# Optimization experiments

Hardware: AMD Instinct MI355X
Metric: run time of the kernel (lower is better)

Reference implementation:

```python
import jax, jax.numpy as jnp
import numpy as np

B, N, D = 4, 2048, 1024
H, HD = 16, 64          # heads, head dim
ROT = 64                # rotary dims (full head)
SCALE = HD ** -0.5


def _rotate_half(x):
    # interleaved pair rotation: (c r) with r=2 -> (-x2, x1)
    x = x.reshape(x.shape[:-1] + (-1, 2))
    x1, x2 = x[..., 0], x[..., 1]
    return jnp.stack((-x2, x1), axis=-1).reshape(x.shape[:-2] + (-1,))


def _rope(t, pos_enc):
    # t: [b,h,n,c], pos_enc: [1,n,rot] -> broadcast over heads
    pe = pos_enc[:, None, : t.shape[-2], :]          # [1,1,n,rot]
    t_rot, t_pass = t[..., :ROT], t[..., ROT:]
    t_rot = t_rot * jnp.cos(pe) + _rotate_half(t_rot) * jnp.sin(pe)
    return jnp.concatenate((t_rot, t_pass), axis=-1)


def setup_inputs() -> dict:
    key = jax.random.key(0)
    ks = jax.random.split(key, 16)
    s = 0.02
    return {
        "query": jax.random.normal(ks[0], (B, N, D), jnp.float32),
        "key": jax.random.normal(ks[1], (B, N, D), jnp.float32),
        "value": jax.random.normal(ks[2], (B, N, D), jnp.float32),
        "pad_mask": jax.random.randint(ks[3], (B, N), 0, 2) > 0,
        "pos_enc": jax.random.uniform(ks[4], (1, N, ROT), jnp.float32),
        "Wq": jax.random.normal(ks[5], (D, D), jnp.float32) * s,
        "bq": jnp.zeros((D,), jnp.float32),
        "Wk": jax.random.normal(ks[6], (D, D), jnp.float32) * s,
        "bk": jnp.zeros((D,), jnp.float32),
        "Wv": jax.random.normal(ks[7], (D, D), jnp.float32) * s,
        "bv": jnp.zeros((D,), jnp.float32),
        "Wo": jax.random.normal(ks[8], (D, D), jnp.float32) * s,
        "bo": jnp.zeros((D,), jnp.float32),
    }


def reference(query, key, value, pad_mask, pos_enc, Wq, bq, Wk, bk, Wv, bv, Wo, bo):
    def split_heads(x):
        return x.reshape(x.shape[0], x.shape[1], H, HD).transpose(0, 2, 1, 3)  # b h n c

    q = split_heads(query @ Wq + bq) * SCALE
    k = split_heads(key @ Wk + bk)
    v = split_heads(value @ Wv + bv)

    q = _rope(q, pos_enc)
    k = _rope(k, pos_enc)

    attn = jnp.einsum("bhic,bhjc->bhij", q, k)
    neg = -jnp.finfo(attn.dtype).max
    attn = jnp.where(pad_mask[:, None, None, :], neg, attn)
    attn = jax.nn.softmax(attn, axis=-1)

    o = jnp.einsum("bhij,bhjc->bhic", attn, v)
    o = o.transpose(0, 2, 1, 3).reshape(o.shape[0], o.shape[2], H * HD)  # b n (h c)
    return o @ Wo + bo
```

## Files before the change

### kernel.cpp

```cpp
#include <hip/hip_runtime.h>

#define B_ 4
#define N_ 2048
#define D_ 1024
#define H_ 16
#define HD_ 64
#define QSCALE_ 0.18033688011112042f

typedef __bf16 bf16x8 __attribute__((ext_vector_type(8)));
typedef float f32x4 __attribute__((ext_vector_type(4)));

#if __has_builtin(__builtin_amdgcn_exp2f)
#define EXP2(x) __builtin_amdgcn_exp2f(x)
#else
#define EXP2(x) exp2f(x)
#endif

__device__ __forceinline__ f32x4 mfma16(bf16x8 a, bf16x8 b, f32x4 c) {
    return __builtin_amdgcn_mfma_f32_16x16x32_bf16(a, b, c, 0, 0, 0);
}

__device__ __forceinline__ void gload16(const void* g, void* l) {
    __builtin_amdgcn_global_load_lds(
        (const __attribute__((address_space(1))) void*)g,
        (__attribute__((address_space(3))) void*)l, 16, 0, 0);
}

__device__ __forceinline__ unsigned pack2(float x, float y) {
    __bf16 a = (__bf16)x, b = (__bf16)y;
    unsigned ua = __builtin_bit_cast(unsigned short, a);
    unsigned ub = __builtin_bit_cast(unsigned short, b);
    return ua | (ub << 16);
}

__global__ __launch_bounds__(256) void pre_kernel(
    const float* __restrict__ q, const float* __restrict__ k, const float* __restrict__ v,
    __bf16* __restrict__ xb,
    const float* __restrict__ W0, const float* __restrict__ W1,
    const float* __restrict__ W2, const float* __restrict__ W3,
    __bf16* __restrict__ T0, __bf16* __restrict__ T1,
    __bf16* __restrict__ T2, __bf16* __restrict__ T3,
    const float* __restrict__ pe, const int* __restrict__ mask,
    unsigned* __restrict__ cstab, float* __restrict__ maskf)
{
    const int y = blockIdx.y;
    const int x = blockIdx.x;
    const int t = threadIdx.x;

    if (y < 3) {
        const float* src = (y == 0) ? q : (y == 1) ? k : v;
        __bf16* dst = xb + (size_t)y * 8388608;
        size_t i = ((size_t)x * 256 + t) * 8;
        float4 a = *(const float4*)(src + i);
        float4 b = *(const float4*)(src + i + 4);
        bf16x8 o;
        o[0] = (__bf16)a.x; o[1] = (__bf16)a.y; o[2] = (__bf16)a.z; o[3] = (__bf16)a.w;
        o[4] = (__bf16)b.x; o[5] = (__bf16)b.y; o[6] = (__bf16)b.z; o[7] = (__bf16)b.w;
        *(bf16x8*)(dst + i) = o;
        return;
    }
    if (x < 1024) {
        const int which = x >> 8;
        const float* W = (which == 0) ? W0 : (which == 1) ? W1 : (which == 2) ? W2 : W3;
        __bf16* Wt = (which == 0) ? T0 : (which == 1) ? T1 : (which == 2) ? T2 : T3;
        const int k0 = ((x >> 4) & 15) * 64, n0 = (x & 15) * 64;
        __shared__ float T[64][65];
#pragma unroll
        for (int i = 0; i < 4; ++i) {
            int row = i * 16 + (t >> 4);
            int c4 = (t & 15) * 4;
            float4 vv = *(const float4*)(W + (size_t)(k0 + row) * D_ + n0 + c4);
            T[row][c4] = vv.x; T[row][c4 + 1] = vv.y; T[row][c4 + 2] = vv.z; T[row][c4 + 3] = vv.w;
        }
        __syncthreads();
#pragma unroll
        for (int i = 0; i < 2; ++i) {
            int task = i * 256 + t;
            int nrow = task >> 3, ks = task & 7;
            bf16x8 o;
#pragma unroll
            for (int e = 0; e < 8; ++e) o[e] = (__bf16)T[ks * 8 + e][nrow];
            *(bf16x8*)(Wt + (size_t)(n0 + nrow) * D_ + k0 + ks * 8) = o;
        }
        return;
    }
    if (x < 1568) {
        int i = (x - 1024) * 256 + t;
        if (i < N_ * HD_) {
            float vv = pe[i];
            __bf16 cb = (__bf16)cosf(vv), sb = (__bf16)sinf(vv);
            unsigned cu = __builtin_bit_cast(unsigned short, cb);
            unsigned su = __builtin_bit_cast(unsigned short, sb);
            cstab[i] = cu | (su << 16);
        }
        if (i < B_ * N_) maskf[i] = mask[i] ? -1e30f : 0.0f;
    }
}

__global__ void prep_kernel(const float* __restrict__ pe, const int* __restrict__ mask,
                            unsigned* __restrict__ cstab, float* __restrict__ maskf) {
    int i = blockIdx.x * 256 + threadIdx.x;
    if (i < N_ * HD_) {
        float v = pe[i];
        __bf16 cb = (__bf16)cosf(v), sb = (__bf16)sinf(v);
        unsigned cu = __builtin_bit_cast(unsigned short, cb);
        unsigned su = __builtin_bit_cast(unsigned short, sb);
        cstab[i] = cu | (su << 16);
    }
    if (i < B_ * N_) maskf[i] = mask[i] ? -1e30f : 0.0f;
}

__global__ __launch_bounds__(256) void tw_kernel(const float* __restrict__ W, __bf16* __restrict__ Wt) {
    __shared__ float T[64][65];
    const int k0 = blockIdx.x * 64, n0 = blockIdx.y * 64;
    const int t = threadIdx.x;
#pragma unroll
    for (int i = 0; i < 4; ++i) {
        int row = i * 16 + (t >> 4);
        int c4 = (t & 15) * 4;
        float4 v = *(const float4*)(W + (size_t)(k0 + row) * D_ + n0 + c4);
        T[row][c4] = v.x; T[row][c4 + 1] = v.y; T[row][c4 + 2] = v.z; T[row][c4 + 3] = v.w;
    }
    __syncthreads();
#pragma unroll
    for (int i = 0; i < 2; ++i) {
        int task = i * 256 + t;
        int nrow = task >> 3, ks = task & 7;
        bf16x8 o;
#pragma unroll
        for (int e = 0; e < 8; ++e) o[e] = (__bf16)T[ks * 8 + e][nrow];
        *(bf16x8*)(Wt + (size_t)(n0 + nrow) * D_ + k0 + ks * 8) = o;
    }
}

__global__ __launch_bounds__(256) void tw3_kernel(
    const float* __restrict__ W0, const float* __restrict__ W1, const float* __restrict__ W2,
    __bf16* __restrict__ T0, __bf16* __restrict__ T1, __bf16* __restrict__ T2)
{
    const float* W = (blockIdx.z == 0) ? W0 : (blockIdx.z == 1) ? W1 : W2;
    __bf16* Wt = (blockIdx.z == 0) ? T0 : (blockIdx.z == 1) ? T1 : T2;
    __shared__ float T[64][65];
    const int k0 = blockIdx.x * 64, n0 = blockIdx.y * 64;
    const int t = threadIdx.x;
#pragma unroll
    for (int i = 0; i < 4; ++i) {
        int row = i * 16 + (t >> 4);
        int c4 = (t & 15) * 4;
        float4 v = *(const float4*)(W + (size_t)(k0 + row) * D_ + n0 + c4);
        T[row][c4] = v.x; T[row][c4 + 1] = v.y; T[row][c4 + 2] = v.z; T[row][c4 + 3] = v.w;
    }
    __syncthreads();
#pragma unroll
    for (int i = 0; i < 2; ++i) {
        int task = i * 256 + t;
        int nrow = task >> 3, ks = task & 7;
        bf16x8 o;
#pragma unroll
        for (int e = 0; e < 8; ++e) o[e] = (__bf16)T[ks * 8 + e][nrow];
        *(bf16x8*)(Wt + (size_t)(n0 + nrow) * D_ + k0 + ks * 8) = o;
    }
}

__global__ __launch_bounds__(256) void proj_v6(
    const __bf16* __restrict__ Xb,
    const __bf16* __restrict__ WtQ, const __bf16* __restrict__ WtK, const __bf16* __restrict__ WtV,
    const float* __restrict__ bQ, const float* __restrict__ bK, const float* __restrict__ bV,
    const unsigned* __restrict__ cstab,
    __bf16* __restrict__ dq, __bf16* __restrict__ dk, __bf16* __restrict__ dv)
{
    __shared__ __align__(16) char smem[35072];
    __bf16* As = (__bf16*)smem;
    __bf16* Bs = (__bf16*)(smem + 16384);

    const int which = blockIdx.y >> 3;
    const __bf16* X   = Xb + (size_t)which * 8388608;
    const __bf16* Wt  = (which == 0) ? WtQ : (which == 1) ? WtK : WtV;
    const float* bias = (which == 0) ? bQ  : (which == 1) ? bK  : bV;
    __bf16* dst       = (which == 0) ? dq  : (which == 1) ? dk  : dv;
    const int mode = which;

    const int tid = threadIdx.x;
    const int lane = tid & 63, w = tid >> 6;
    const int wr = w >> 1, wc = w & 1;
    const int r16 = lane & 15, g = lane >> 4;
    const int m0 = blockIdx.x * 128;
    const int n0 = (blockIdx.y & 7) * 128;
    const int srow8 = tid >> 3, slot = tid & 7;

    f32x4 acc[4][4];
#pragma unroll
    for (int m = 0; m < 4; ++m)
#pragma unroll
        for (int n = 0; n < 4; ++n) acc[m][n] = (f32x4){0.f, 0.f, 0.f, 0.f};

    for (int kt = 0; kt < 16; ++kt) {
#pragma unroll
        for (int j = 0; j < 4; ++j) {
            int row = j * 32 + srow8;
            const char* srcA = (const char*)X + ((size_t)(m0 + row) * D_ + kt * 64) * 2
                               + ((slot ^ (row & 7)) << 4);
            gload16(srcA, (char*)As + j * 4096 + w * 1024);
            const char* srcB = (const char*)Wt + ((size_t)(n0 + row) * D_ + kt * 64) * 2
                               + ((slot ^ (row & 7)) << 4);
            gload16(srcB, (char*)Bs + j * 4096 + w * 1024);
        }
        __syncthreads();
#pragma unroll
        for (int kk = 0; kk < 2; ++kk) {
            bf16x8 aF[4], bF[4];
#pragma unroll
            for (int m = 0; m < 4; ++m) {
                int row = wr * 64 + m * 16 + r16;
                aF[m] = *(const bf16x8*)((char*)As + row * 128 + (((kk * 4 + g) ^ (row & 7)) << 4));
            }
#pragma unroll
            for (int n = 0; n < 4; ++n) {
                int row = wc * 64 + n * 16 + r16;
                bF[n] = *(const bf16x8*)((char*)Bs + row * 128 + (((kk * 4 + g) ^ (row & 7)) << 4));
            }
#pragma unroll
            for (int m = 0; m < 4; ++m)
#pragma unroll
                for (int n = 0; n < 4; ++n)
                    acc[m][n] = mfma16(aF[m], bF[n], acc[m][n]);
        }
        __syncthreads();
    }

    if (mode <= 1) {
#pragma unroll
        for (int m = 0; m < 4; ++m)
#pragma unroll
            for (int n = 0; n < 4; ++n) {
                int col = n0 + wc * 64 + n * 16 + r16;
                int h = col >> 6, hd = col & 63;
#pragma unroll
                for (int j = 0; j < 4; ++j) {
                    int bn = m0 + wr * 64 + m * 16 + g * 4 + j;
                    int np = bn & (N_ - 1), b = bn >> 11;
                    float val = acc[m][n][j] + bias[col];
                    if (mode == 0) val *= QSCALE_;
                    float other = __shfl_xor(val, 1);
                    unsigned cs = cstab[np * HD_ + hd];
                    float c = __uint_as_float(cs << 16);
                    float sn = __uint_as_float(cs & 0xffff0000u);
                    val = val * c + ((col & 1) ? other : -other) * sn;
                    dst[((size_t)(b * H_ + h) * N_ + np) * HD_ + hd] = (__bf16)val;
                }
            }
    } else {
        __bf16* T = (__bf16*)smem;
        __syncthreads();
#pragma unroll
        for (int m = 0; m < 4; ++m)
#pragma unroll
            for (int n = 0; n < 4; ++n) {
                int c = wc * 64 + n * 16 + r16;
                float bs = bias[n0 + c];
#pragma unroll
                for (int j = 0; j < 4; ++j) {
                    int sr = wr * 64 + m * 16 + g * 4 + j;
                    T[c * 136 + sr] = (__bf16)(acc[m][n][j] + bs);
                }
            }
        __syncthreads();
        const int b = m0 >> 11, np0 = m0 & (N_ - 1);
#pragma unroll
        for (int i = 0; i < 8; ++i) {
            int task = i * 256 + tid;
            int trow = task >> 4, ch = task & 15;
            int colg = n0 + trow;
            int h = colg >> 6, hd = colg & 63;
            bf16x8 vv = *(const bf16x8*)&T[trow * 136 + ch * 8];
            *(bf16x8*)(dst + (((size_t)(b * H_ + h) * HD_ + hd) * N_ + np0 + ch * 8)) = vv;
        }
    }
}

__global__ __launch_bounds__(256) void proj_v5(
    const float* __restrict__ Xq, const float* __restrict__ Xk, const float* __restrict__ Xv,
    const __bf16* __restrict__ WtQ, const __bf16* __restrict__ WtK, const __bf16* __restrict__ WtV,
    const float* __restrict__ bQ, const float* __restrict__ bK, const float* __restrict__ bV,
    const unsigned* __restrict__ cstab,
    __bf16* __restrict__ dq, __bf16* __restrict__ dk, __bf16* __restrict__ dv)
{
    __shared__ __align__(16) char smem[35072];
    __bf16* As = (__bf16*)smem;
    __bf16* Bs = (__bf16*)(smem + 16384);

    const int which = blockIdx.y >> 3;
    const float* X    = (which == 0) ? Xq  : (which == 1) ? Xk  : Xv;
    const __bf16* Wt  = (which == 0) ? WtQ : (which == 1) ? WtK : WtV;
    const float* bias = (which == 0) ? bQ  : (which == 1) ? bK  : bV;
    __bf16* dst       = (which == 0) ? dq  : (which == 1) ? dk  : dv;
    const int mode = which;

    const int tid = threadIdx.x;
    const int lane = tid & 63, w = tid >> 6;
    const int wr = w >> 1, wc = w & 1;
    const int r16 = lane & 15, g = lane >> 4;
    const int m0 = blockIdx.x * 128;
    const int n0 = (blockIdx.y & 7) * 128;
    const int srow8 = tid >> 3, slot = tid & 7;

    f32x4 acc[4][4];
#pragma unroll
    for (int m = 0; m < 4; ++m)
#pragma unroll
        for (int n = 0; n < 4; ++n) acc[m][n] = (f32x4){0.f, 0.f, 0.f, 0.f};

    for (int kt = 0; kt < 16; ++kt) {
        float4 va0[4], va1[4];
#pragma unroll
        for (int i = 0; i < 4; ++i) {
            int row = i * 32 + srow8;
            const float* s = X + (size_t)(m0 + row) * D_ + kt * 64 + slot * 8;
            va0[i] = *(const float4*)s;
            va1[i] = *(const float4*)(s + 4);
        }
#pragma unroll
        for (int j = 0; j < 4; ++j) {
            int row = j * 32 + srow8;
            const char* src = (const char*)Wt + ((size_t)(n0 + row) * D_ + kt * 64) * 2
                              + ((slot ^ (row & 7)) << 4);
            gload16(src, (char*)Bs + j * 4096 + w * 1024);
        }
#pragma unroll
        for (int i = 0; i < 4; ++i) {
            int row = i * 32 + srow8;
            bf16x8 bv;
            bv[0] = (__bf16)va0[i].x; bv[1] = (__bf16)va0[i].y;
            bv[2] = (__bf16)va0[i].z; bv[3] = (__bf16)va0[i].w;
            bv[4] = (__bf16)va1[i].x; bv[5] = (__bf16)va1[i].y;
            bv[6] = (__bf16)va1[i].z; bv[7] = (__bf16)va1[i].w;
            *(bf16x8*)((char*)As + row * 128 + ((slot ^ (row & 7)) << 4)) = bv;
        }
        __syncthreads();
#pragma unroll
        for (int kk = 0; kk < 2; ++kk) {
            bf16x8 aF[4], bF[4];
#pragma unroll
            for (int m = 0; m < 4; ++m) {
                int row = wr * 64 + m * 16 + r16;
                aF[m] = *(const bf16x8*)((char*)As + row * 128 + (((kk * 4 + g) ^ (row & 7)) << 4));
            }
#pragma unroll
            for (int n = 0; n < 4; ++n) {
                int row = wc * 64 + n * 16 + r16;
                bF[n] = *(const bf16x8*)((char*)Bs + row * 128 + (((kk * 4 + g) ^ (row & 7)) << 4));
            }
#pragma unroll
            for (int m = 0; m < 4; ++m)
#pragma unroll
                for (int n = 0; n < 4; ++n)
                    acc[m][n] = mfma16(aF[m], bF[n], acc[m][n]);
        }
        __syncthreads();
    }

    if (mode <= 1) {
#pragma unroll
        for (int m = 0; m < 4; ++m)
#pragma unroll
            for (int n = 0; n < 4; ++n) {
                int col = n0 + wc * 64 + n * 16 + r16;
                int h = col >> 6, hd = col & 63;
#pragma unroll
                for (int j = 0; j < 4; ++j) {
                    int bn = m0 + wr * 64 + m * 16 + g * 4 + j;
                    int np = bn & (N_ - 1), b = bn >> 11;
                    float val = acc[m][n][j] + bias[col];
                    if (mode == 0) val *= QSCALE_;
                    float other = __shfl_xor(val, 1);
                    unsigned cs = cstab[np * HD_ + hd];
                    float c = __uint_as_float(cs << 16);
                    float sn = __uint_as_float(cs & 0xffff0000u);
                    val = val * c + ((col & 1) ? other : -other) * sn;
                    dst[((size_t)(b * H_ + h) * N_ + np) * HD_ + hd] = (__bf16)val;
                }
            }
    } else {
        __bf16* T = (__bf16*)smem;
        __syncthreads();
#pragma unroll
        for (int m = 0; m < 4; ++m)
#pragma unroll
            for (int n = 0; n < 4; ++n) {
                int c = wc * 64 + n * 16 + r16;
                float bs = bias[n0 + c];
#pragma unroll
                for (int j = 0; j < 4; ++j) {
                    int sr = wr * 64 + m * 16 + g * 4 + j;
                    T[c * 136 + sr] = (__bf16)(acc[m][n][j] + bs);
                }
            }
        __syncthreads();
        const int b = m0 >> 11, np0 = m0 & (N_ - 1);
#pragma unroll
        for (int i = 0; i < 8; ++i) {
            int task = i * 256 + tid;
            int trow = task >> 4, ch = task & 15;
            int colg = n0 + trow;
            int h = colg >> 6, hd = colg & 63;
            bf16x8 vv = *(const bf16x8*)&T[trow * 136 + ch * 8];
            *(bf16x8*)(dst + (((size_t)(b * H_ + h) * HD_ + hd) * N_ + np0 + ch * 8)) = vv;
        }
    }
}

__global__ __launch_bounds__(256, 4) void attn_v7(
    const __bf16* __restrict__ qws, const __bf16* __restrict__ kws,
    const __bf16* __restrict__ vtws, const float* __restrict__ maskf,
    __bf16* __restrict__ ows)
{
    __shared__ __align__(16) __bf16 Ks0[4096], Ks1[4096];
    __shared__ __align__(16) __bf16 Vs0[4096], Vs1[4096];
    __shared__ __align__(16) char Pbuf[8192];

    const int tid = threadIdx.x;
    const int lane = tid & 63, w = tid >> 6;
    const int r16 = lane & 15, g = lane >> 4;

    const int lid = blockIdx.x;
    const int virt = (lid & 7) * 128 + (lid >> 3);
    const int bh = virt >> 4;
    const int b = bh >> 4, h = bh & 15;
    const int q0 = (virt & 15) * 128;
    const int srow8 = tid >> 3, slot = tid & 7;

    bf16x8 qF[2][2];
#pragma unroll
    for (int qq = 0; qq < 2; ++qq) {
        const __bf16* qb = qws + ((size_t)bh * N_ + q0 + w * 32 + qq * 16 + r16) * HD_ + g * 8;
        qF[qq][0] = *(const bf16x8*)qb;
        qF[qq][1] = *(const bf16x8*)(qb + 32);
    }

    bf16x8 onesF;
#pragma unroll
    for (int e = 0; e < 8; ++e) onesF[e] = (__bf16)1.0f;

    const char* kbase = (const char*)(kws + (size_t)bh * N_ * HD_);
    const char* vbase = (const char*)(vtws + (size_t)bh * HD_ * N_);
    const float* mbase = maskf + b * N_;
    char* Pw = Pbuf + w * 2048;

    f32x4 o[2][4];
    f32x4 lacc[2];
#pragma unroll
    for (int qq = 0; qq < 2; ++qq) {
        lacc[qq] = (f32x4){0.f, 0.f, 0.f, 0.f};
#pragma unroll
        for (int n = 0; n < 4; ++n) o[qq][n] = (f32x4){0.f, 0.f, 0.f, 0.f};
    }

#define STAGE_(KD, VD, kt) {                                                          \
    _Pragma("unroll")                                                                 \
    for (int j = 0; j < 2; ++j) {                                                     \
        int row = j * 32 + srow8;                                                     \
        gload16(kbase + (size_t)((kt) * 64 + row) * 128 + ((slot ^ (row & 7)) << 4),  \
                (char*)(KD) + j * 4096 + w * 1024);                                   \
    }                                                                                 \
    _Pragma("unroll")                                                                 \
    for (int j = 0; j < 2; ++j) {                                                     \
        int row = j * 32 + srow8;                                                     \
        gload16(vbase + (size_t)row * (N_ * 2) + (kt) * 128 + ((slot ^ (row & 7)) << 4), \
                (char*)(VD) + j * 4096 + w * 1024);                                   \
    } }

#define TILE_(KB, VB, KN, VN, kt) {                                                   \
    if ((kt) + 1 < 32) STAGE_(KN, VN, (kt) + 1);                                      \
    f32x4 s0[4], s1[4];                                                               \
    _Pragma("unroll")                                                                 \
    for (int n = 0; n < 4; ++n) {                                                     \
        f32x4 mb = *(const f32x4*)(mbase + (kt) * 64 + n * 16 + g * 4);               \
        s0[n] = mb; s1[n] = mb;                                                       \
    }                                                                                 \
    __builtin_amdgcn_s_setprio(1);                                                    \
    _Pragma("unroll")                                                                 \
    for (int n = 0; n < 4; ++n) {                                                     \
        int row = n * 16 + r16;                                                       \
        bf16x8 kF0 = *(const bf16x8*)((const char*)(KB) + row * 128 + ((g ^ (row & 7)) << 4));        \
        bf16x8 kF1 = *(const bf16x8*)((const char*)(KB) + row * 128 + (((4 + g) ^ (row & 7)) << 4));  \
        s0[n] = mfma16(kF0, qF[0][0], s0[n]);                                         \
        s0[n] = mfma16(kF1, qF[0][1], s0[n]);                                         \
        s1[n] = mfma16(kF0, qF[1][0], s1[n]);                                         \
        s1[n] = mfma16(kF1, qF[1][1], s1[n]);                                         \
    }                                                                                 \
    __builtin_amdgcn_s_setprio(0);                                                    \
    bf16x8 pF0[2], pF1[2];                                                            \
                                                                       \
    _Pragma("unroll")                                                                 \
    for (int n = 0; n < 4; ++n) {                                                     \
        int u0 = ((n * 2 + (g >> 1)) ^ (r16 & 7));                                    \
        int off = (g & 1) * 2;                                                        \
        *(unsigned*)(Pw + r16 * 128 + u0 * 16 + off * 4)       = pack2(EXP2(s0[n][0]), EXP2(s0[n][1])); \
        *(unsigned*)(Pw + r16 * 128 + u0 * 16 + (off + 1) * 4) = pack2(EXP2(s0[n][2]), EXP2(s0[n][3])); \
    }                                                                                 \
    _Pragma("unroll")                                                                 \
    for (int kk = 0; kk < 2; ++kk)                                                    \
        pF0[kk] = *(const bf16x8*)(Pw + r16 * 128 + (((kk * 4 + g) ^ (r16 & 7)) << 4)); \
                                       \
    __builtin_amdgcn_s_setprio(1);                                                    \
    _Pragma("unroll")                                                                 \
    for (int n = 0; n < 4; ++n) {                                                     \
        int row = n * 16 + r16;                                                       \
        bf16x8 vF0 = *(const bf16x8*)((const char*)(VB) + row * 128 + ((g ^ (row & 7)) << 4));        \
        bf16x8 vF1 = *(const bf16x8*)((const char*)(VB) + row * 128 + (((4 + g) ^ (row & 7)) << 4));  \
        o[0][n] = mfma16(vF0, pF0[0], o[0][n]);                                       \
        o[0][n] = mfma16(vF1, pF0[1], o[0][n]);                                       \
    }                                                                                 \
    __builtin_amdgcn_s_setprio(0);                                                    \
                                                                       \
    _Pragma("unroll")                                                                 \
    for (int n = 0; n < 4; ++n) {                                                     \
        int u0 = ((n * 2 + (g >> 1)) ^ (r16 & 7));                                    \
        int off = (g & 1) * 2;                                                        \
        *(unsigned*)(Pw + r16 * 128 + u0 * 16 + off * 4)       = pack2(EXP2(s1[n][0]), EXP2(s1[n][1])); \
        *(unsigned*)(Pw + r16 * 128 + u0 * 16 + (off + 1) * 4) = pack2(EXP2(s1[n][2]), EXP2(s1[n][3])); \
    }                                                                                 \
    _Pragma("unroll")                                                                 \
    for (int kk = 0; kk < 2; ++kk)                                                    \
        pF1[kk] = *(const bf16x8*)(Pw + r16 * 128 + (((kk * 4 + g) ^ (r16 & 7)) << 4)); \
                                                                       \
    __builtin_amdgcn_s_setprio(1);                                                    \
    _Pragma("unroll")                                                                 \
    for (int n = 0; n < 4; ++n) {                                                     \
        int row = n * 16 + r16;                                                       \
        bf16x8 vF0 = *(const bf16x8*)((const char*)(VB) + row * 128 + ((g ^ (row & 7)) << 4));        \
        bf16x8 vF1 = *(const bf16x8*)((const char*)(VB) + row * 128 + (((4 + g) ^ (row & 7)) << 4));  \
        o[1][n] = mfma16(vF0, pF1[0], o[1][n]);                                       \
        o[1][n] = mfma16(vF1, pF1[1], o[1][n]);                                       \
    }                                                                                 \
                \
    lacc[0] = mfma16(onesF, pF0[0], lacc[0]);                                         \
    lacc[0] = mfma16(onesF, pF0[1], lacc[0]);                                         \
    lacc[1] = mfma16(onesF, pF1[0], lacc[1]);                                         \
    lacc[1] = mfma16(onesF, pF1[1], lacc[1]);                                         \
    __builtin_amdgcn_s_setprio(0);                                                    \
    __syncthreads(); }

    STAGE_(Ks0, Vs0, 0);
    __syncthreads();

    for (int kt = 0; kt < 32; kt += 2) {
        TILE_(Ks0, Vs0, Ks1, Vs1, kt);
        TILE_(Ks1, Vs1, Ks0, Vs0, kt + 1);
    }
#undef TILE_
#undef STAGE_

#pragma unroll
    for (int qq = 0; qq < 2; ++qq) {
        float inv = 1.0f / lacc[qq][0];
#pragma unroll
        for (int n = 0; n < 4; ++n) {
            int u0 = ((n * 2 + (g >> 1)) ^ (r16 & 7));
            int off = (g & 1) * 2;
            *(unsigned*)(Pw + r16 * 128 + u0 * 16 + off * 4)       = pack2(o[qq][n][0] * inv, o[qq][n][1] * inv);
            *(unsigned*)(Pw + r16 * 128 + u0 * 16 + (off + 1) * 4) = pack2(o[qq][n][2] * inv, o[qq][n][3] * inv);
        }
        int qrow = q0 + w * 32 + qq * 16 + r16;
#pragma unroll
        for (int kk = 0; kk < 2; ++kk) {
            bf16x8 v = *(const bf16x8*)(Pw + r16 * 128 + (((kk * 4 + g) ^ (r16 & 7)) << 4));
            *(bf16x8*)(ows + ((size_t)(b * N_ + qrow)) * D_ + h * HD_ + kk * 32 + g * 8) = v;
        }
    }
}

__global__ __launch_bounds__(256) void gemm_out_v2(
    const __bf16* __restrict__ A, const __bf16* __restrict__ Wt,
    const float* __restrict__ bias, float* __restrict__ out)
{
    __shared__ __align__(16) __bf16 As[8192], Bs[8192];

    const int tid = threadIdx.x;
    const int lane = tid & 63, w = tid >> 6;
    const int wr = w >> 1, wc = w & 1;
    const int r16 = lane & 15, g = lane >> 4;
    const int m0 = blockIdx.x * 128;
    const int n0 = blockIdx.y * 128;
    const int srow8 = tid >> 3, slot = tid & 7;

    f32x4 acc[4][4];
#pragma unroll
    for (int m = 0; m < 4; ++m)
#pragma unroll
        for (int n = 0; n < 4; ++n) acc[m][n] = (f32x4){0.f, 0.f, 0.f, 0.f};

    for (int kt = 0; kt < 16; ++kt) {
#pragma unroll
        for (int j = 0; j < 4; ++j) {
            int row = j * 32 + srow8;
            const char* srcA = (const char*)A + ((size_t)(m0 + row) * D_ + kt * 64) * 2
                               + ((slot ^ (row & 7)) << 4);
            gload16(srcA, (char*)As + j * 4096 + w * 1024);
            const char* srcB = (const char*)Wt + ((size_t)(n0 + row) * D_ + kt * 64) * 2
                               + ((slot ^ (row & 7)) << 4);
            gload16(srcB, (char*)Bs + j * 4096 + w * 1024);
        }
        __syncthreads();
#pragma unroll
        for (int kk = 0; kk < 2; ++kk) {
            bf16x8 aF[4], bF[4];
#pragma unroll
            for (int m = 0; m < 4; ++m) {
                int row = wr * 64 + m * 16 + r16;
                aF[m] = *(const bf16x8*)((char*)As + row * 128 + (((kk * 4 + g) ^ (row & 7)) << 4));
            }
#pragma unroll
            for (int n = 0; n < 4; ++n) {
                int row = wc * 64 + n * 16 + r16;
                bF[n] = *(const bf16x8*)((char*)Bs + row * 128 + (((kk * 4 + g) ^ (row & 7)) << 4));
            }
#pragma unroll
            for (int m = 0; m < 4; ++m)
#pragma unroll
                for (int n = 0; n < 4; ++n)
                    acc[m][n] = mfma16(aF[m], bF[n], acc[m][n]);
        }
        __syncthreads();
    }

#pragma unroll
    for (int m = 0; m < 4; ++m)
#pragma unroll
        for (int n = 0; n < 4; ++n) {
            int col = n0 + wc * 64 + n * 16 + r16;
            float bs = bias[col];
#pragma unroll
            for (int j = 0; j < 4; ++j) {
                int bn = m0 + wr * 64 + m * 16 + g * 4 + j;
                out[(size_t)bn * D_ + col] = acc[m][n][j] + bs;
            }
        }
}

extern "C" void kernel_launch(void* const* d_in, const int* in_sizes, int n_in,
                              void* d_out, int out_size, void* d_ws, size_t ws_size,
                              hipStream_t stream)
{
    const float* query = (const float*)d_in[0];
    const float* key   = (const float*)d_in[1];
    const float* value = (const float*)d_in[2];
    const int* mask    = (const int*)d_in[3];
    const float* pos_enc = (const float*)d_in[4];
    const float* Wq = (const float*)d_in[5];
    const float* bq = (const float*)d_in[6];
    const float* Wk = (const float*)d_in[7];
    const float* bk = (const float*)d_in[8];
    const float* Wv = (const float*)d_in[9];
    const float* bv = (const float*)d_in[10];
    const float* Wo = (const float*)d_in[11];
    const float* bo = (const float*)d_in[12];
    float* out = (float*)d_out;

    char* ws = (char*)d_ws;
    const size_t MB16 = (size_t)16 * 1024 * 1024;
    const size_t MB2  = (size_t)2 * 1024 * 1024;
    const size_t need_big = 3 * MB16 + 4 * MB16 + 4 * MB2 + 524288 + 32768;
    const size_t need_small = 4 * MB16 + 524288 + 32768;

    if (ws_size >= need_big) {
        __bf16* Xb    = (__bf16*)(ws);
        __bf16* qws   = (__bf16*)(ws + 3 * MB16);
        __bf16* kws   = (__bf16*)(ws + 4 * MB16);
        __bf16* vtws  = (__bf16*)(ws + 5 * MB16);
        __bf16* ows   = (__bf16*)(ws + 6 * MB16);
        __bf16* wtQ   = (__bf16*)(ws + 7 * MB16);
        __bf16* wtK   = (__bf16*)(ws + 7 * MB16 + MB2);
        __bf16* wtV   = (__bf16*)(ws + 7 * MB16 + 2 * MB2);
        __bf16* wtO   = (__bf16*)(ws + 7 * MB16 + 3 * MB2);
        unsigned* cstab = (unsigned*)(ws + 7 * MB16 + 4 * MB2);
        float* maskf  = (float*)(ws + 7 * MB16 + 4 * MB2 + 524288);

        hipLaunchKernelGGL(pre_kernel, dim3(4096, 4), dim3(256), 0, stream,
                           query, key, value, Xb, Wq, Wk, Wv, Wo, wtQ, wtK, wtV, wtO,
                           pos_enc, mask, cstab, maskf);
        hipLaunchKernelGGL(proj_v6, dim3(64, 24), dim3(256), 0, stream,
                           Xb, wtQ, wtK, wtV, bq, bk, bv, cstab, qws, kws, vtws);
        hipLaunchKernelGGL(attn_v7, dim3(1024), dim3(256), 0, stream,
                           qws, kws, vtws, maskf, ows);
        hipLaunchKernelGGL(gemm_out_v2, dim3(64, 8), dim3(256), 0, stream, ows, wtO, bo, out);
    } else {
        if (ws_size < need_small) return;
        __bf16* qws   = (__bf16*)(ws);
        __bf16* kws   = (__bf16*)(ws + MB16);
        __bf16* vtws  = (__bf16*)(ws + 2 * MB16);
        __bf16* ows   = (__bf16*)(ws + 3 * MB16);
        unsigned* cstab = (unsigned*)(ws + 4 * MB16);
        float* maskf  = (float*)(ws + 4 * MB16 + 524288);
        __bf16* wtQ   = (__bf16*)(ws + 3 * MB16);
        __bf16* wtK   = wtQ + (size_t)D_ * D_;
        __bf16* wtV   = wtK + (size_t)D_ * D_;
        __bf16* wtO   = (__bf16*)(ws);

        hipLaunchKernelGGL(prep_kernel, dim3(512), dim3(256), 0, stream, pos_enc, mask, cstab, maskf);
        hipLaunchKernelGGL(tw3_kernel, dim3(16, 16, 3), dim3(256), 0, stream, Wq, Wk, Wv, wtQ, wtK, wtV);
        hipLaunchKernelGGL(proj_v5, dim3(64, 24), dim3(256), 0, stream,
                           query, key, value, wtQ, wtK, wtV, bq, bk, bv, cstab, qws, kws, vtws);
        hipLaunchKernelGGL(attn_v7, dim3(1024), dim3(256), 0, stream,
                           qws, kws, vtws, maskf, ows);
        hipLaunchKernelGGL(tw_kernel, dim3(16, 16), dim3(256), 0, stream, Wo, wtO);
        hipLaunchKernelGGL(gemm_out_v2, dim3(64, 8), dim3(256), 0, stream, ows, wtO, bo, out);
    }
}
```

Baseline: 217.1 us.

## Use 512-thread attention blocks covering 256 queries to share K/V tiles

The attention kernel now runs 8 waves per block, each block covering 256 query rows instead of 128, so every staged K/V tile in shared memory serves twice as many queries. Staging is split across all 512 threads with one load each per K and V. The P·V MFMAs for both query sub-tiles are merged into a single loop that reuses each V fragment read, and the row-sum MFMAs are moved earlier. The cost is a larger P buffer, fewer blocks, and possibly lower occupancy under the 512-thread launch bound.

New measurement: 206.4 us, median of 2. 4.9% less time.

```diff
diff --git a/kernel.cpp b/kernel.cpp
--- a/kernel.cpp
+++ b/kernel.cpp
@@ -408,24 +408,24 @@
     }
 }
 
-__global__ __launch_bounds__(256, 4) void attn_v7(
+__global__ __launch_bounds__(512, 4) void attn_v8(
     const __bf16* __restrict__ qws, const __bf16* __restrict__ kws,
     const __bf16* __restrict__ vtws, const float* __restrict__ maskf,
     __bf16* __restrict__ ows)
 {
     __shared__ __align__(16) __bf16 Ks0[4096], Ks1[4096];
     __shared__ __align__(16) __bf16 Vs0[4096], Vs1[4096];
-    __shared__ __align__(16) char Pbuf[8192];
+    __shared__ __align__(16) char Pbuf[16384];
 
     const int tid = threadIdx.x;
     const int lane = tid & 63, w = tid >> 6;
     const int r16 = lane & 15, g = lane >> 4;
 
     const int lid = blockIdx.x;
-    const int virt = (lid & 7) * 128 + (lid >> 3);
-    const int bh = virt >> 4;
+    const int virt = (lid & 7) * 64 + (lid >> 3);
+    const int bh = virt >> 3;
     const int b = bh >> 4, h = bh & 15;
-    const int q0 = (virt & 15) * 128;
+    const int q0 = (virt & 7) * 256;
     const int srow8 = tid >> 3, slot = tid & 7;
 
     bf16x8 qF[2][2];
@@ -455,18 +455,11 @@
     }
 
 #define STAGE_(KD, VD, kt) {                                                          \
-    _Pragma("unroll")                                                                 \
-    for (int j = 0; j < 2; ++j) {                                                     \
-        int row = j * 32 + srow8;                                                     \
-        gload16(kbase + (size_t)((kt) * 64 + row) * 128 + ((slot ^ (row & 7)) << 4),  \
-                (char*)(KD) + j * 4096 + w * 1024);                                   \
-    }                                                                                 \
-    _Pragma("unroll")                                                                 \
-    for (int j = 0; j < 2; ++j) {                                                     \
-        int row = j * 32 + srow8;                                                     \
-        gload16(vbase + (size_t)row * (N_ * 2) + (kt) * 128 + ((slot ^ (row & 7)) << 4), \
-                (char*)(VD) + j * 4096 + w * 1024);                                   \
-    } }
+    gload16(kbase + (size_t)((kt) * 64 + srow8) * 128 + ((slot ^ (srow8 & 7)) << 4),  \
+            (char*)(KD) + w * 1024);                                                  \
+    gload16(vbase + (size_t)srow8 * (N_ * 2) + (kt) * 128 + ((slot ^ (srow8 & 7)) << 4), \
+            (char*)(VD) + w * 1024);                                                  \
+    }
 
 #define TILE_(KB, VB, KN, VN, kt) {                                                   \
     if ((kt) + 1 < 32) STAGE_(KN, VN, (kt) + 1);                                      \
@@ -489,7 +482,6 @@
     }                                                                                 \
     __builtin_amdgcn_s_setprio(0);                                                    \
     bf16x8 pF0[2], pF1[2];                                                            \
-                                                                       \
     _Pragma("unroll")                                                                 \
     for (int n = 0; n < 4; ++n) {                                                     \
         int u0 = ((n * 2 + (g >> 1)) ^ (r16 & 7));                                    \
@@ -500,18 +492,8 @@
     _Pragma("unroll")                                                                 \
     for (int kk = 0; kk < 2; ++kk)                                                    \
         pF0[kk] = *(const bf16x8*)(Pw + r16 * 128 + (((kk * 4 + g) ^ (r16 & 7)) << 4)); \
-                                       \
-    __builtin_amdgcn_s_setprio(1);                                                    \
-    _Pragma("unroll")                                                                 \
-    for (int n = 0; n < 4; ++n) {                                                     \
-        int row = n * 16 + r16;                                                       \
-        bf16x8 vF0 = *(const bf16x8*)((const char*)(VB) + row * 128 + ((g ^ (row & 7)) << 4));        \
-        bf16x8 vF1 = *(const bf16x8*)((const char*)(VB) + row * 128 + (((4 + g) ^ (row & 7)) << 4));  \
-        o[0][n] = mfma16(vF0, pF0[0], o[0][n]);                                       \
-        o[0][n] = mfma16(vF1, pF0[1], o[0][n]);                                       \
-    }                                                                                 \
-    __builtin_amdgcn_s_setprio(0);                                                    \
-                                                                       \
+    lacc[0] = mfma16(onesF, pF0[0], lacc[0]);                                         \
+    lacc[0] = mfma16(onesF, pF0[1], lacc[0]);                                         \
     _Pragma("unroll")                                                                 \
     for (int n = 0; n < 4; ++n) {                                                     \
         int u0 = ((n * 2 + (g >> 1)) ^ (r16 & 7));                                    \
@@ -522,21 +504,19 @@
     _Pragma("unroll")                                                                 \
     for (int kk = 0; kk < 2; ++kk)                                                    \
         pF1[kk] = *(const bf16x8*)(Pw + r16 * 128 + (((kk * 4 + g) ^ (r16 & 7)) << 4)); \
-                                                                       \
+    lacc[1] = mfma16(onesF, pF1[0], lacc[1]);                                         \
+    lacc[1] = mfma16(onesF, pF1[1], lacc[1]);                                         \
     __builtin_amdgcn_s_setprio(1);                                                    \
     _Pragma("unroll")                                                                 \
     for (int n = 0; n < 4; ++n) {                                                     \
         int row = n * 16 + r16;                                                       \
         bf16x8 vF0 = *(const bf16x8*)((const char*)(VB) + row * 128 + ((g ^ (row & 7)) << 4));        \
         bf16x8 vF1 = *(const bf16x8*)((const char*)(VB) + row * 128 + (((4 + g) ^ (row & 7)) << 4));  \
+        o[0][n] = mfma16(vF0, pF0[0], o[0][n]);                                       \
+        o[0][n] = mfma16(vF1, pF0[1], o[0][n]);                                       \
         o[1][n] = mfma16(vF0, pF1[0], o[1][n]);                                       \
         o[1][n] = mfma16(vF1, pF1[1], o[1][n]);                                       \
     }                                                                                 \
-                \
-    lacc[0] = mfma16(onesF, pF0[0], lacc[0]);                                         \
-    lacc[0] = mfma16(onesF, pF0[1], lacc[0]);                                         \
-    lacc[1] = mfma16(onesF, pF1[0], lacc[1]);                                         \
-    lacc[1] = mfma16(onesF, pF1[1], lacc[1]);                                         \
     __builtin_amdgcn_s_setprio(0);                                                    \
     __syncthreads(); }
 
@@ -680,7 +660,7 @@
                            pos_enc, mask, cstab, maskf);
         hipLaunchKernelGGL(proj_v6, dim3(64, 24), dim3(256), 0, stream,
                            Xb, wtQ, wtK, wtV, bq, bk, bv, cstab, qws, kws, vtws);
-        hipLaunchKernelGGL(attn_v7, dim3(1024), dim3(256), 0, stream,
+        hipLaunchKernelGGL(attn_v8, dim3(512), dim3(512), 0, stream,
                            qws, kws, vtws, maskf, ows);
         hipLaunchKernelGGL(gemm_out_v2, dim3(64, 8), dim3(256), 0, stream, ows, wtO, bo, out);
     } else {
@@ -700,7 +680,7 @@
         hipLaunchKernelGGL(tw3_kernel, dim3(16, 16, 3), dim3(256), 0, stream, Wq, Wk, Wv, wtQ, wtK, wtV);
         hipLaunchKernelGGL(proj_v5, dim3(64, 24), dim3(256), 0, stream,
                            query, key, value, wtQ, wtK, wtV, bq, bk, bv, cstab, qws, kws, vtws);
-        hipLaunchKernelGGL(attn_v7, dim3(1024), dim3(256), 0, stream,
+        hipLaunchKernelGGL(attn_v8, dim3(512), dim3(512), 0, stream,
                            qws, kws, vtws, maskf, ows);
         hipLaunchKernelGGL(tw_kernel, dim3(16, 16), dim3(256), 0, stream, Wo, wtO);
         hipLaunchKernelGGL(gemm_out_v2, dim3(64, 8), dim3(256), 0, stream, ows, wtO, bo, out);
```
